# Kernel optimization log

Measured on AMD Instinct MI355X. Metric: run time of the kernel, lower is better.

Reference implementation:

```python
import jax, jax.numpy as jnp
import numpy as np

B, N, H, NH = 2, 2048, 1024, 16
HD = H // NH


def setup_inputs() -> dict:
    key = jax.random.key(0)
    ks = jax.random.split(key, 12)
    s = 0.02
    inp = {
        "q": jax.random.normal(ks[0], (B, N, H), jnp.float32),
        "k": jax.random.normal(ks[1], (B, N, H), jnp.float32),
        "v": jax.random.normal(ks[2], (B, N, H), jnp.float32),
        # causal mask, broadcast over batch and heads
        "mask": jnp.tril(jnp.ones((N, N), jnp.float32))[None, None, :, :],
        "Wq": jax.random.normal(ks[3], (H, H), jnp.float32) * s,
        "bq": jnp.zeros((H,), jnp.float32),
        "Wk": jax.random.normal(ks[4], (H, H), jnp.float32) * s,
        "bk": jnp.zeros((H,), jnp.float32),
        "Wv": jax.random.normal(ks[5], (H, H), jnp.float32) * s,
        "bv": jnp.zeros((H,), jnp.float32),
        "Wp": jax.random.normal(ks[6], (H, H), jnp.float32) * s,
        "bp": jnp.zeros((H,), jnp.float32),
    }
    return inp


def _split_heads(x):
    # [b, n, (h d)] -> [b, h, n, d]
    b, n, _ = x.shape
    return x.reshape(b, n, NH, HD).transpose(0, 2, 1, 3)


def reference(q, k, v, mask, Wq, bq, Wk, bk, Wv, bv, Wp, bp):
    Q = _split_heads(q @ Wq.T + bq)                      # [b,h,n,d]
    K = _split_heads(k @ Wk.T + bk)
    V = _split_heads(v @ Wv.T + bv)
    scores = jnp.einsum("bhnd,bhmd->bhnm", Q, K) / jnp.sqrt(jnp.float32(HD))
    scores = jnp.where(mask == 0, -jnp.inf, scores)
    attn = jax.nn.softmax(scores, axis=-1)
    out = jnp.einsum("bhnm,bhmd->bhnd", attn, V)         # [b,h,n,d]
    out = out.transpose(0, 2, 1, 3).reshape(q.shape[0], q.shape[1], H)
    # dropout is identity in eval mode
    return out @ Wp.T + bp
```

## Files before the change

### kernel.cpp

```cpp
#include <hip/hip_runtime.h>


typedef unsigned short ushortT;
typedef unsigned int uintT;
typedef __attribute__((ext_vector_type(8))) short short8;
typedef __attribute__((ext_vector_type(4))) float f32x4;

#define M_ROWS 4096
#define KDIM   1024
#define NDIM   1024
#define SEQ    2048
#define HDHEAD 64

__device__ __forceinline__ float bf2f(ushortT s) {
    union { unsigned u; float f; } v; v.u = ((unsigned)s) << 16; return v.f;
}
__device__ __forceinline__ ushortT f2bf(float x) {
    union { float f; unsigned u; } v; v.f = x;
    return (ushortT)((v.u + 0x7fffu + ((v.u >> 16) & 1u)) >> 16);
}

__device__ __forceinline__ bool detect_f32(const uintT* w) {
    int hits = 0;
#pragma unroll
    for (int i = 0; i < 16; ++i) {
        const unsigned e = (w[i] >> 7) & 0xffu;
        hits += (e >= 118u && e <= 131u) ? 1 : 0;
    }
    return hits < 8;
}

__device__ __forceinline__ short8 cvt8(const float* p) {
    f32x4 a = *(const f32x4*)p;
    f32x4 b = *(const f32x4*)(p + 4);
    short8 r;
    r[0] = (short)f2bf(a[0]); r[1] = (short)f2bf(a[1]);
    r[2] = (short)f2bf(a[2]); r[3] = (short)f2bf(a[3]);
    r[4] = (short)f2bf(b[0]); r[5] = (short)f2bf(b[1]);
    r[6] = (short)f2bf(b[2]); r[7] = (short)f2bf(b[3]);
    return r;
}

__device__ __forceinline__ void gl2lds16(const ushortT* g, ushortT* l) {
    __builtin_amdgcn_global_load_lds(
        (const __attribute__((address_space(1))) void*)g,
        (__attribute__((address_space(3))) void*)l,
        16, 0, 0);
}

__global__ __launch_bounds__(256) void convert_kernel(
    const void* __restrict__ q, const void* __restrict__ k, const void* __restrict__ v,
    const void* __restrict__ Wq, const void* __restrict__ Wk,
    const void* __restrict__ Wv, const void* __restrict__ Wp,
    const void* __restrict__ bq, const void* __restrict__ bk,
    const void* __restrict__ bv, const void* __restrict__ bp,
    ushortT* __restrict__ dst) {
    const bool f32m = detect_f32((const uintT*)q);
    const size_t u = (size_t)blockIdx.x * 256 + threadIdx.x;

    const void* src; size_t soff, doff;
    if (u < 1572864u) {
        const int seg = (int)(u >> 19);
        const size_t o = u & 524287u;
        src  = seg == 0 ? q : (seg == 1 ? k : v);
        soff = o * 8;
        doff = (size_t)seg * 4194304u + o * 8;
    } else if (u < 2097152u) {
        const size_t u2 = u - 1572864u;
        const int seg = (int)(u2 >> 17);
        const size_t o = u2 & 131071u;
        src  = seg == 0 ? Wq : (seg == 1 ? Wk : (seg == 2 ? Wv : Wp));
        soff = o * 8;
        doff = 12582912u + (size_t)seg * 1048576u + o * 8;
    } else {
        const size_t u3 = u - 2097152u;
        const int seg = (int)(u3 >> 7);
        const size_t o = u3 & 127u;
        src  = seg == 0 ? bq : (seg == 1 ? bk : (seg == 2 ? bv : bp));
        soff = o * 8;
        doff = 16777216u + (size_t)seg * 1024u + o * 8;
    }

    if (f32m)
        *(short8*)(dst + doff) = cvt8((const float*)src + soff);
    else
        *(short8*)(dst + doff) = *(const short8*)((const ushortT*)src + soff);
}

__device__ __forceinline__ void gemm_body(const void* __restrict__ Av,
                                          const void* __restrict__ Wv_,
                                          const void* __restrict__ biasv,
                                          void* __restrict__ Cv,
                                          bool a_f32, bool w_f32, bool c_f32,
                                          float cscale, bool vt_store) {
    __shared__ ushortT ldsA[128 * 64];
    __shared__ ushortT ldsB[128 * 64];

    const int tid  = threadIdx.x;
    const int lane = tid & 63;
    const int wid  = tid >> 6;
    const int bm   = blockIdx.x;
    const int bn   = blockIdx.y;
    const int wm   = wid >> 1;
    const int wn   = wid & 1;

    const int srow = lane >> 2;
    const int scol = (lane & 3) * 8;

    f32x4 acc[4][4];
#pragma unroll
    for (int i = 0; i < 4; ++i)
#pragma unroll
        for (int j = 0; j < 4; ++j) acc[i][j] = (f32x4){0.f, 0.f, 0.f, 0.f};

    const int fr   = lane & 15;
    const int quad = lane >> 4;

    for (int kt = 0; kt < KDIM / 64; ++kt) {
        const int k0 = kt * 64;
        if (!a_f32 && !w_f32) {
#pragma unroll
            for (int t = 0; t < 4; ++t) {
                const int chunk = wid * 4 + t;
                const int kh  = chunk >> 3;
                const int r16 = (chunk & 7) * 16;
                const size_t ra = (size_t)(bm * 128 + r16 + srow) * KDIM + k0 + kh * 32 + scol;
                const size_t rw = (size_t)(bn * 128 + r16 + srow) * KDIM + k0 + kh * 32 + scol;
                gl2lds16((const ushortT*)Av + ra, ldsA + chunk * 512);
                gl2lds16((const ushortT*)Wv_ + rw, ldsB + chunk * 512);
            }
        } else {
            short8 ta[4], tb[4];
#pragma unroll
            for (int t = 0; t < 4; ++t) {
                const int chunk = wid * 4 + t;
                const int kh  = chunk >> 3;
                const int r16 = (chunk & 7) * 16;
                const size_t ra = (size_t)(bm * 128 + r16 + srow) * KDIM + k0 + kh * 32 + scol;
                const size_t rw = (size_t)(bn * 128 + r16 + srow) * KDIM + k0 + kh * 32 + scol;
                ta[t] = a_f32 ? cvt8((const float*)Av + ra)
                              : *(const short8*)((const ushortT*)Av + ra);
                tb[t] = w_f32 ? cvt8((const float*)Wv_ + rw)
                              : *(const short8*)((const ushortT*)Wv_ + rw);
            }
#pragma unroll
            for (int t = 0; t < 4; ++t) {
                const int chunk = wid * 4 + t;
                *(short8*)(ldsA + chunk * 512 + lane * 8) = ta[t];
                *(short8*)(ldsB + chunk * 512 + lane * 8) = tb[t];
            }
        }
        __syncthreads();

#pragma unroll
        for (int s = 0; s < 2; ++s) {
            short8 aF[4], bF[4];
#pragma unroll
            for (int i = 0; i < 4; ++i)
                aF[i] = *(const short8*)(ldsA + s * 4096 + (wm * 64 + i * 16 + fr) * 32 + quad * 8);
#pragma unroll
            for (int j = 0; j < 4; ++j)
                bF[j] = *(const short8*)(ldsB + s * 4096 + (wn * 64 + j * 16 + fr) * 32 + quad * 8);
#pragma unroll
            for (int i = 0; i < 4; ++i)
#pragma unroll
                for (int j = 0; j < 4; ++j)
                    acc[i][j] = __builtin_amdgcn_mfma_f32_16x16x32_bf16(aF[i], bF[j], acc[i][j], 0, 0, 0);
        }
        __syncthreads();
    }

#pragma unroll
    for (int j = 0; j < 4; ++j) {
        const int col = bn * 128 + wn * 64 + j * 16 + fr;
        const float bv = w_f32 ? ((const float*)biasv)[col]
                               : bf2f(((const ushortT*)biasv)[col]);
#pragma unroll
        for (int i = 0; i < 4; ++i) {
            const int row0 = bm * 128 + wm * 64 + i * 16 + quad * 4;
#pragma unroll
            for (int r = 0; r < 4; ++r) {
                const float val = (acc[i][j][r] + bv) * cscale;
                const int row = row0 + r;
                if (vt_store) {
                    const int bb = row >> 11, n = row & 2047;
                    const int hh = col >> 6,  d = col & 63;
                    ((ushortT*)Cv)[(size_t)((bb * 16 + hh) * 64 + d) * SEQ + n] = f2bf(val);
                } else if (c_f32) {
                    ((float*)Cv)[(size_t)row * NDIM + col] = val;
                } else {
                    ((ushortT*)Cv)[(size_t)row * NDIM + col] = f2bf(val);
                }
            }
        }
    }
}

__global__ __launch_bounds__(256, 2) void qkv_proj_kernel(
    const void* __restrict__ q, const void* __restrict__ k, const void* __restrict__ v,
    const void* __restrict__ Wq, const void* __restrict__ Wk, const void* __restrict__ Wv,
    const void* __restrict__ bq, const void* __restrict__ bk, const void* __restrict__ bv,
    ushortT* __restrict__ Qp, ushortT* __restrict__ Kp, ushortT* __restrict__ Vt) {
    const bool f32m = detect_f32((const uintT*)q);
    const void* A; const void* W; const void* bias; ushortT* C;
    float cscale = 1.f; bool vt = false;
    if (blockIdx.z == 0)      { A = q; W = Wq; bias = bq; C = Qp; cscale = 0.125f; }
    else if (blockIdx.z == 1) { A = k; W = Wk; bias = bk; C = Kp; }
    else                      { A = v; W = Wv; bias = bv; C = Vt; vt = true; }
    gemm_body(A, W, bias, (void*)C, f32m, f32m, false, cscale, vt);
}

__global__ __launch_bounds__(256, 2) void out_proj_kernel(
    const ushortT* __restrict__ A, const void* __restrict__ W,
    const void* __restrict__ bias, void* __restrict__ C,
    const void* __restrict__ qdet) {
    const bool wf = detect_f32((const uintT*)W);
    const bool cf = detect_f32((const uintT*)qdet);
    gemm_body((const void*)A, W, bias, C, false, wf, cf, 1.f, false);
}

template <int SPLIT>
__global__ __launch_bounds__(256, SPLIT ? 4 : 2) void flash_attn_kernel(
    const ushortT* __restrict__ Qp, const ushortT* __restrict__ Kp,
    const ushortT* __restrict__ Vt, ushortT* __restrict__ Ob) {
    __shared__ ushortT ldsK[2 * 64 * 40];
    __shared__ ushortT ldsV[64 * 72];
    __shared__ ushortT ldsP[4][16 * 72];

    const int tid  = threadIdx.x;
    const int lane = tid & 63;
    const int wid  = tid >> 6;
    const int fr   = lane & 15;
    const int quad = lane >> 4;

    int pid, sp;
    if constexpr (SPLIT) { pid = blockIdx.x & 15; sp = blockIdx.x >> 4; }
    else                 { pid = blockIdx.x;      sp = 0; }
    const int kstep = SPLIT ? 2 : 1;
    const int h = blockIdx.y;
    const int b = blockIdx.z;

    const size_t base  = (size_t)b * SEQ * NDIM + (size_t)h * HDHEAD;
    const size_t vtb   = (size_t)(b * 16 + h) * HDHEAD * SEQ;

    int ksst[2], keyloc[2];
#pragma unroll
    for (int t = 0; t < 2; ++t) {
        const int chunk = wid * 2 + t;
        ksst[t]   = chunk >> 2;
        keyloc[t] = (chunk & 3) * 16 + (lane >> 2);
    }
    const int c8 = (lane & 3) * 8;
    const int vd  = lane >> 3;
    const int vk8 = (lane & 7) * 8;

    for (int half = 0; half < 2; ++half) {
        const int qb = (half == 0) ? pid : (31 - pid);
        const int q0 = qb * 64;
        const int nkv = qb + 1;

        short8 qf[2];
#pragma unroll
        for (int ks = 0; ks < 2; ++ks)
            qf[ks] = *(const short8*)(Qp + base + (size_t)(q0 + wid * 16 + fr) * NDIM + ks * 32 + quad * 8);

        f32x4 accO[4];
#pragma unroll
        for (int dt = 0; dt < 4; ++dt) accO[dt] = (f32x4){0.f, 0.f, 0.f, 0.f};
        float lsum[4];
#pragma unroll
        for (int r = 0; r < 4; ++r) lsum[r] = 0.f;

        short8 kreg[2], vreg[2];
        const int kvp = sp * 64;
#pragma unroll
        for (int t = 0; t < 2; ++t) {
            kreg[t] = *(const short8*)(Kp + base + (size_t)(kvp + keyloc[t]) * NDIM + ksst[t] * 32 + c8);
            const int d = (wid * 2 + t) * 8 + vd;
            vreg[t] = *(const short8*)(Vt + vtb + (size_t)d * SEQ + kvp + vk8);
        }

        for (int kt = sp; kt < nkv; kt += kstep) {
            __syncthreads();

#pragma unroll
            for (int t = 0; t < 2; ++t) {
                *(short8*)(ldsK + ksst[t] * 2560 + keyloc[t] * 40 + c8) = kreg[t];
                const int d = (wid * 2 + t) * 8 + vd;
                *(short8*)(ldsV + d * 72 + vk8) = vreg[t];
            }

            if (kt + kstep < nkv) {
                const int kv1 = (kt + kstep) * 64;
#pragma unroll
                for (int t = 0; t < 2; ++t) {
                    kreg[t] = *(const short8*)(Kp + base + (size_t)(kv1 + keyloc[t]) * NDIM + ksst[t] * 32 + c8);
                    const int d = (wid * 2 + t) * 8 + vd;
                    vreg[t] = *(const short8*)(Vt + vtb + (size_t)d * SEQ + kv1 + vk8);
                }
            }
            __syncthreads();

            f32x4 s[4];
#pragma unroll
            for (int nt = 0; nt < 4; ++nt) {
                f32x4 a = (f32x4){0.f, 0.f, 0.f, 0.f};
#pragma unroll
                for (int ks = 0; ks < 2; ++ks) {
                    short8 kf = *(const short8*)(ldsK + ks * 2560 + (nt * 16 + fr) * 40 + quad * 8);
                    a = __builtin_amdgcn_mfma_f32_16x16x32_bf16(qf[ks], kf, a, 0, 0, 0);
                }
                s[nt] = a;
            }

            const int kv0 = kt * 64;
            const int qi = q0 + wid * 16 + quad * 4;
            if (kt == nkv - 1) {
#pragma unroll
                for (int nt = 0; nt < 4; ++nt) {
                    const int kj = kv0 + nt * 16 + fr;
#pragma unroll
                    for (int r = 0; r < 4; ++r)
                        s[nt][r] = (kj > qi + r) ? -1e30f : s[nt][r];
                }
            }

            ushortT* pbuf = ldsP[wid];
#pragma unroll
            for (int nt = 0; nt < 4; ++nt) {
#pragma unroll
                for (int r = 0; r < 4; ++r) {
                    const float p = __expf(fminf(s[nt][r], 30.f));
                    lsum[r] += p;
                    pbuf[(quad * 4 + r) * 72 + nt * 16 + fr] = f2bf(p);
                }
            }

            asm volatile("" ::: "memory");

#pragma unroll
            for (int ks = 0; ks < 2; ++ks) {
                short8 pf = *(const short8*)(pbuf + fr * 72 + ks * 32 + quad * 8);
#pragma unroll
                for (int dt = 0; dt < 4; ++dt) {
                    short8 vf = *(const short8*)(ldsV + (dt * 16 + fr) * 72 + ks * 32 + quad * 8);
                    accO[dt] = __builtin_amdgcn_mfma_f32_16x16x32_bf16(pf, vf, accO[dt], 0, 0, 0);
                }
            }
        }

#pragma unroll
        for (int r = 0; r < 4; ++r) {
#pragma unroll
            for (int off = 8; off >= 1; off >>= 1)
                lsum[r] += __shfl_xor(lsum[r], off, 64);
        }

        if constexpr (SPLIT) {
            const size_t pofs = ((size_t)((sp * 2 + b) * 16 + h)) * SEQ * 72;
#pragma unroll
            for (int dt = 0; dt < 4; ++dt) {
#pragma unroll
                for (int r = 0; r < 4; ++r) {
                    const size_t row = (size_t)(q0 + wid * 16 + quad * 4 + r);
                    Ob[pofs + row * 72 + dt * 16 + fr] = f2bf(accO[dt][r]);
                }
            }
            if (fr == 0) {
#pragma unroll
                for (int r = 0; r < 4; ++r) {
                    const size_t row = (size_t)(q0 + wid * 16 + quad * 4 + r);
                    *(float*)(Ob + pofs + row * 72 + 64) = lsum[r];
                }
            }
        } else {
#pragma unroll
            for (int dt = 0; dt < 4; ++dt) {
#pragma unroll
                for (int r = 0; r < 4; ++r) {
                    const size_t row = (size_t)(q0 + wid * 16 + quad * 4 + r);
                    Ob[(size_t)b * SEQ * NDIM + row * NDIM + h * HDHEAD + dt * 16 + fr] =
                        f2bf(accO[dt][r] / lsum[r]);
                }
            }
        }
    }
}

__global__ __launch_bounds__(256) void combine_kernel(
    const ushortT* __restrict__ Part, ushortT* __restrict__ Op) {
    const uintT u = blockIdx.x * 256 + threadIdx.x;
    const int d8  = u & 7;
    const int h   = (u >> 3) & 15;
    const int row = (u >> 7) & 2047;
    const int b   = (int)(u >> 18);

    const size_t r0 = (((size_t)((0 + b) * 16 + h)) * SEQ + row) * 72;
    const size_t r1 = (((size_t)((2 + b) * 16 + h)) * SEQ + row) * 72;
    const short8 p0 = *(const short8*)(Part + r0 + d8 * 8);
    const short8 p1 = *(const short8*)(Part + r1 + d8 * 8);
    const float l = *(const float*)(Part + r0 + 64) + *(const float*)(Part + r1 + 64);
    const float inv = 1.f / l;

    short8 o;
#pragma unroll
    for (int i = 0; i < 8; ++i)
        o[i] = (short)f2bf((bf2f((ushortT)p0[i]) + bf2f((ushortT)p1[i])) * inv);

    Op[((size_t)b * SEQ + row) * NDIM + h * HDHEAD + d8 * 8 + 0] = 0;
    *(short8*)(Op + ((size_t)b * SEQ + row) * NDIM + h * HDHEAD + d8 * 8) = o;
}

extern "C" void kernel_launch(void* const* d_in, const int* in_sizes, int n_in,
                              void* d_out, int out_size, void* d_ws, size_t ws_size,
                              hipStream_t stream) {
    const void* q  = d_in[0];
    const void* k  = d_in[1];
    const void* v  = d_in[2];
    const void* Wq = d_in[4];
    const void* bq = d_in[5];
    const void* Wk = d_in[6];
    const void* bk = d_in[7];
    const void* Wv = d_in[8];
    const void* bv = d_in[9];
    const void* Wp = d_in[10];
    const void* bp = d_in[11];

    dim3 blk(256);
    const size_t FAST_WS = 58728448;

    if (ws_size >= FAST_WS) {
        ushortT* cb   = (ushortT*)d_ws;
        ushortT* qb16 = cb;
        ushortT* kb16 = cb + 4194304u;
        ushortT* vb16 = cb + 8388608u;
        ushortT* Wqb  = cb + 12582912u;
        ushortT* Wkb  = cb + 13631488u;
        ushortT* Wvb  = cb + 14680064u;
        ushortT* Wpb  = cb + 15728640u;
        ushortT* bqb  = cb + 16777216u;
        ushortT* bkb  = cb + 16778240u;
        ushortT* bvb  = cb + 16779264u;
        ushortT* bpb  = cb + 16780288u;
        ushortT* Qp   = cb + 16781312u;
        ushortT* Kp   = Qp + 4194304u;
        ushortT* Vt   = Kp + 4194304u;
        ushortT* Part = cb;
        ushortT* Op   = Vt;

        convert_kernel<<<dim3(8194), blk, 0, stream>>>(
            q, k, v, Wq, Wk, Wv, Wp, bq, bk, bv, bp, cb);
        qkv_proj_kernel<<<dim3(32, 8, 3), blk, 0, stream>>>(
            qb16, kb16, vb16, Wqb, Wkb, Wvb, bqb, bkb, bvb, Qp, Kp, Vt);
        flash_attn_kernel<1><<<dim3(32, 16, 2), blk, 0, stream>>>(Qp, Kp, Vt, Part);
        combine_kernel<<<dim3(2048), blk, 0, stream>>>(Part, Op);
        out_proj_kernel<<<dim3(32, 8), blk, 0, stream>>>(Op, Wpb, bpb, d_out, q);
    } else {
        ushortT* ws = (ushortT*)d_ws;
        ushortT* Qp = ws;
        ushortT* Kp = ws + (size_t)M_ROWS * NDIM;
        ushortT* Vt = ws + (size_t)2 * M_ROWS * NDIM;
        ushortT* Op = ws + (size_t)3 * M_ROWS * NDIM;

        qkv_proj_kernel<<<dim3(32, 8, 3), blk, 0, stream>>>(
            q, k, v, Wq, Wk, Wv, bq, bk, bv, Qp, Kp, Vt);
        flash_attn_kernel<0><<<dim3(16, 16, 2), blk, 0, stream>>>(Qp, Kp, Vt, Op);
        out_proj_kernel<<<dim3(32, 8), blk, 0, stream>>>(Op, Wp, bp, d_out, q);
    }
}
```

Baseline: 247.5 us.

## Compute transposed S tiles per key slice so P stores are vectorized

Each warp now holds one 16-key slice of K and computes S^T against all 64 query rows, so the exponentiated P values pack into 4-wide vector stores into a block-shared P buffer. This replaces the scattered scalar per-warp P writes. It adds a block-wide barrier before the PV product and a cross-warp row-sum reduction through LDS, and each thread now keeps all Q fragments in registers. A redundant scalar store in the combine kernel is also removed.

```diff
diff --git a/kernel.cpp b/kernel.cpp
--- a/kernel.cpp
+++ b/kernel.cpp
@@ -4,6 +4,7 @@
 typedef unsigned short ushortT;
 typedef unsigned int uintT;
 typedef __attribute__((ext_vector_type(8))) short short8;
+typedef __attribute__((ext_vector_type(4))) short short4v;
 typedef __attribute__((ext_vector_type(4))) float f32x4;
 
 #define M_ROWS 4096
@@ -225,7 +226,8 @@
     const ushortT* __restrict__ Vt, ushortT* __restrict__ Ob) {
     __shared__ ushortT ldsK[2 * 64 * 40];
     __shared__ ushortT ldsV[64 * 72];
-    __shared__ ushortT ldsP[4][16 * 72];
+    __shared__ ushortT ldsP[64 * 72];
+    __shared__ float   ldsL[4][64];
 
     const int tid  = threadIdx.x;
     const int lane = tid & 63;
@@ -259,17 +261,19 @@
         const int q0 = qb * 64;
         const int nkv = qb + 1;
 
-        short8 qf[2];
-#pragma unroll
-        for (int ks = 0; ks < 2; ++ks)
-            qf[ks] = *(const short8*)(Qp + base + (size_t)(q0 + wid * 16 + fr) * NDIM + ks * 32 + quad * 8);
+        short8 qf[4][2];
+#pragma unroll
+        for (int i = 0; i < 4; ++i)
+#pragma unroll
+            for (int ks = 0; ks < 2; ++ks)
+                qf[i][ks] = *(const short8*)(Qp + base + (size_t)(q0 + i * 16 + fr) * NDIM + ks * 32 + quad * 8);
 
         f32x4 accO[4];
 #pragma unroll
         for (int dt = 0; dt < 4; ++dt) accO[dt] = (f32x4){0.f, 0.f, 0.f, 0.f};
-        float lsum[4];
-#pragma unroll
-        for (int r = 0; r < 4; ++r) lsum[r] = 0.f;
+        float ls[4];
+#pragma unroll
+        for (int i = 0; i < 4; ++i) ls[i] = 0.f;
 
         short8 kreg[2], vreg[2];
         const int kvp = sp * 64;
@@ -301,46 +305,50 @@
             }
             __syncthreads();
 
-            f32x4 s[4];
-#pragma unroll
-            for (int nt = 0; nt < 4; ++nt) {
+            short8 kf[2];
+#pragma unroll
+            for (int ks = 0; ks < 2; ++ks)
+                kf[ks] = *(const short8*)(ldsK + ks * 2560 + (wid * 16 + fr) * 40 + quad * 8);
+
+            f32x4 st[4];
+#pragma unroll
+            for (int i = 0; i < 4; ++i) {
                 f32x4 a = (f32x4){0.f, 0.f, 0.f, 0.f};
 #pragma unroll
-                for (int ks = 0; ks < 2; ++ks) {
-                    short8 kf = *(const short8*)(ldsK + ks * 2560 + (nt * 16 + fr) * 40 + quad * 8);
-                    a = __builtin_amdgcn_mfma_f32_16x16x32_bf16(qf[ks], kf, a, 0, 0, 0);
-                }
-                s[nt] = a;
+                for (int ks = 0; ks < 2; ++ks)
+                    a = __builtin_amdgcn_mfma_f32_16x16x32_bf16(kf[ks], qf[i][ks], a, 0, 0, 0);
+                st[i] = a;
             }
 
             const int kv0 = kt * 64;
-            const int qi = q0 + wid * 16 + quad * 4;
             if (kt == nkv - 1) {
-#pragma unroll
-                for (int nt = 0; nt < 4; ++nt) {
-                    const int kj = kv0 + nt * 16 + fr;
+                const int kjb = kv0 + wid * 16 + quad * 4;
+#pragma unroll
+                for (int i = 0; i < 4; ++i) {
+                    const int qi = q0 + i * 16 + fr;
 #pragma unroll
                     for (int r = 0; r < 4; ++r)
-                        s[nt][r] = (kj > qi + r) ? -1e30f : s[nt][r];
-                }
-            }
-
-            ushortT* pbuf = ldsP[wid];
-#pragma unroll
-            for (int nt = 0; nt < 4; ++nt) {
+                        st[i][r] = (kjb + r > qi) ? -1e30f : st[i][r];
+                }
+            }
+
+#pragma unroll
+            for (int i = 0; i < 4; ++i) {
+                short4v pk;
 #pragma unroll
                 for (int r = 0; r < 4; ++r) {
-                    const float p = __expf(fminf(s[nt][r], 30.f));
-                    lsum[r] += p;
-                    pbuf[(quad * 4 + r) * 72 + nt * 16 + fr] = f2bf(p);
-                }
-            }
-
-            asm volatile("" ::: "memory");
+                    const float p = __expf(fminf(st[i][r], 30.f));
+                    ls[i] += p;
+                    pk[r] = (short)f2bf(p);
+                }
+                *(short4v*)(ldsP + (i * 16 + fr) * 72 + wid * 16 + quad * 4) = pk;
+            }
+
+            __syncthreads();
 
 #pragma unroll
             for (int ks = 0; ks < 2; ++ks) {
-                short8 pf = *(const short8*)(pbuf + fr * 72 + ks * 32 + quad * 8);
+                short8 pf = *(const short8*)(ldsP + (wid * 16 + fr) * 72 + ks * 32 + quad * 8);
 #pragma unroll
                 for (int dt = 0; dt < 4; ++dt) {
                     short8 vf = *(const short8*)(ldsV + (dt * 16 + fr) * 72 + ks * 32 + quad * 8);
@@ -350,10 +358,23 @@
         }
 
 #pragma unroll
+        for (int i = 0; i < 4; ++i) {
+            ls[i] += __shfl_xor(ls[i], 16, 64);
+            ls[i] += __shfl_xor(ls[i], 32, 64);
+        }
+        __syncthreads();
+        if (lane < 16) {
+#pragma unroll
+            for (int i = 0; i < 4; ++i)
+                ldsL[wid][i * 16 + lane] = ls[i];
+        }
+        __syncthreads();
+
+        float ltot[4];
+#pragma unroll
         for (int r = 0; r < 4; ++r) {
-#pragma unroll
-            for (int off = 8; off >= 1; off >>= 1)
-                lsum[r] += __shfl_xor(lsum[r], off, 64);
+            const int qrow = wid * 16 + quad * 4 + r;
+            ltot[r] = ldsL[0][qrow] + ldsL[1][qrow] + ldsL[2][qrow] + ldsL[3][qrow];
         }
 
         if constexpr (SPLIT) {
@@ -370,7 +391,7 @@
 #pragma unroll
                 for (int r = 0; r < 4; ++r) {
                     const size_t row = (size_t)(q0 + wid * 16 + quad * 4 + r);
-                    *(float*)(Ob + pofs + row * 72 + 64) = lsum[r];
+                    *(float*)(Ob + pofs + row * 72 + 64) = ltot[r];
                 }
             }
         } else {
@@ -380,10 +401,11 @@
                 for (int r = 0; r < 4; ++r) {
                     const size_t row = (size_t)(q0 + wid * 16 + quad * 4 + r);
                     Ob[(size_t)b * SEQ * NDIM + row * NDIM + h * HDHEAD + dt * 16 + fr] =
-                        f2bf(accO[dt][r] / lsum[r]);
-                }
-            }
-        }
+                        f2bf(accO[dt][r] / ltot[r]);
+                }
+            }
+        }
+        __syncthreads();
     }
 }
 
@@ -407,7 +429,6 @@
     for (int i = 0; i < 8; ++i)
         o[i] = (short)f2bf((bf2f((ushortT)p0[i]) + bf2f((ushortT)p1[i])) * inv);
 
-    Op[((size_t)b * SEQ + row) * NDIM + h * HDHEAD + d8 * 8 + 0] = 0;
     *(short8*)(Op + ((size_t)b * SEQ + row) * NDIM + h * HDHEAD + d8 * 8) = o;
 }
 
```

New measurement: 250.5 us. About the same (+1.2%).

## Fuse split-KV combine into output projection GEMM A-tile load

Applied to the files above, without the earlier changes.

Removes the separate combine kernel and instead merges the two split-attention partial outputs, normalising by the summed row sums, while loading A tiles inside a new output projection GEMM kernel. This saves one launch and the write and re-read of the combined attention output. The trade-off is that each of the 8 N-blocks recomputes the combine for its rows, so partial buffers are read 8 times. The A operand is also now staged through registers rather than via direct global-to-LDS loads, and the loop has no double buffering.

```diff
diff --git a/kernel.cpp b/kernel.cpp
--- a/kernel.cpp
+++ b/kernel.cpp
@@ -219,6 +219,105 @@
     gemm_body((const void*)A, W, bias, C, false, wf, cf, 1.f, false);
 }
 
+__global__ __launch_bounds__(256, 2) void out_proj_combined(
+    const ushortT* __restrict__ Part, const ushortT* __restrict__ W,
+    const ushortT* __restrict__ bias, void* __restrict__ C,
+    const void* __restrict__ qdet) {
+    __shared__ ushortT ldsA[128 * 64];
+    __shared__ ushortT ldsB[128 * 64];
+
+    const bool cf = detect_f32((const uintT*)qdet);
+
+    const int tid  = threadIdx.x;
+    const int lane = tid & 63;
+    const int wid  = tid >> 6;
+    const int bm   = blockIdx.x;
+    const int bn   = blockIdx.y;
+    const int wm   = wid >> 1;
+    const int wn   = wid & 1;
+
+    const int srow = lane >> 2;
+    const int scol = (lane & 3) * 8;
+
+    f32x4 acc[4][4];
+#pragma unroll
+    for (int i = 0; i < 4; ++i)
+#pragma unroll
+        for (int j = 0; j < 4; ++j) acc[i][j] = (f32x4){0.f, 0.f, 0.f, 0.f};
+
+    const int fr   = lane & 15;
+    const int quad = lane >> 4;
+
+    for (int kt = 0; kt < KDIM / 64; ++kt) {
+        const int k0 = kt * 64;
+        short8 ta[4];
+#pragma unroll
+        for (int t = 0; t < 4; ++t) {
+            const int chunk = wid * 4 + t;
+            const int kh   = chunk >> 3;
+            const int r16  = (chunk & 7) * 16;
+            const int row  = bm * 128 + r16 + srow;
+            const int bb   = row >> 11;
+            const int row2 = row & 2047;
+            const int c    = k0 + kh * 32 + scol;
+            const int hh   = c >> 6, d = c & 63;
+            const size_t rb0 = (((size_t)(bb * 16 + hh)) * SEQ + row2) * 72;
+            const size_t rb1 = (((size_t)((2 + bb) * 16 + hh)) * SEQ + row2) * 72;
+            const short8 p0 = *(const short8*)(Part + rb0 + d);
+            const short8 p1 = *(const short8*)(Part + rb1 + d);
+            const float l = *(const float*)(Part + rb0 + 64)
+                          + *(const float*)(Part + rb1 + 64);
+            const float inv = 1.f / l;
+            short8 o;
+#pragma unroll
+            for (int i = 0; i < 8; ++i)
+                o[i] = (short)f2bf((bf2f((ushortT)p0[i]) + bf2f((ushortT)p1[i])) * inv);
+            ta[t] = o;
+
+            const size_t rw = (size_t)(bn * 128 + r16 + srow) * KDIM + k0 + kh * 32 + scol;
+            gl2lds16(W + rw, ldsB + chunk * 512);
+        }
+#pragma unroll
+        for (int t = 0; t < 4; ++t)
+            *(short8*)(ldsA + (wid * 4 + t) * 512 + lane * 8) = ta[t];
+        __syncthreads();
+
+#pragma unroll
+        for (int s = 0; s < 2; ++s) {
+            short8 aF[4], bF[4];
+#pragma unroll
+            for (int i = 0; i < 4; ++i)
+                aF[i] = *(const short8*)(ldsA + s * 4096 + (wm * 64 + i * 16 + fr) * 32 + quad * 8);
+#pragma unroll
+            for (int j = 0; j < 4; ++j)
+                bF[j] = *(const short8*)(ldsB + s * 4096 + (wn * 64 + j * 16 + fr) * 32 + quad * 8);
+#pragma unroll
+            for (int i = 0; i < 4; ++i)
+#pragma unroll
+                for (int j = 0; j < 4; ++j)
+                    acc[i][j] = __builtin_amdgcn_mfma_f32_16x16x32_bf16(aF[i], bF[j], acc[i][j], 0, 0, 0);
+        }
+        __syncthreads();
+    }
+
+#pragma unroll
+    for (int j = 0; j < 4; ++j) {
+        const int col = bn * 128 + wn * 64 + j * 16 + fr;
+        const float bv = bf2f(bias[col]);
+#pragma unroll
+        for (int i = 0; i < 4; ++i) {
+            const int row0 = bm * 128 + wm * 64 + i * 16 + quad * 4;
+#pragma unroll
+            for (int r = 0; r < 4; ++r) {
+                const float val = acc[i][j][r] + bv;
+                const int row = row0 + r;
+                if (cf) ((float*)C)[(size_t)row * NDIM + col] = val;
+                else    ((ushortT*)C)[(size_t)row * NDIM + col] = f2bf(val);
+            }
+        }
+    }
+}
+
 template <int SPLIT>
 __global__ __launch_bounds__(256, SPLIT ? 4 : 2) void flash_attn_kernel(
     const ushortT* __restrict__ Qp, const ushortT* __restrict__ Kp,
@@ -385,30 +484,6 @@
             }
         }
     }
-}
-
-__global__ __launch_bounds__(256) void combine_kernel(
-    const ushortT* __restrict__ Part, ushortT* __restrict__ Op) {
-    const uintT u = blockIdx.x * 256 + threadIdx.x;
-    const int d8  = u & 7;
-    const int h   = (u >> 3) & 15;
-    const int row = (u >> 7) & 2047;
-    const int b   = (int)(u >> 18);
-
-    const size_t r0 = (((size_t)((0 + b) * 16 + h)) * SEQ + row) * 72;
-    const size_t r1 = (((size_t)((2 + b) * 16 + h)) * SEQ + row) * 72;
-    const short8 p0 = *(const short8*)(Part + r0 + d8 * 8);
-    const short8 p1 = *(const short8*)(Part + r1 + d8 * 8);
-    const float l = *(const float*)(Part + r0 + 64) + *(const float*)(Part + r1 + 64);
-    const float inv = 1.f / l;
-
-    short8 o;
-#pragma unroll
-    for (int i = 0; i < 8; ++i)
-        o[i] = (short)f2bf((bf2f((ushortT)p0[i]) + bf2f((ushortT)p1[i])) * inv);
-
-    Op[((size_t)b * SEQ + row) * NDIM + h * HDHEAD + d8 * 8 + 0] = 0;
-    *(short8*)(Op + ((size_t)b * SEQ + row) * NDIM + h * HDHEAD + d8 * 8) = o;
 }
 
 extern "C" void kernel_launch(void* const* d_in, const int* in_sizes, int n_in,
@@ -446,15 +521,13 @@
         ushortT* Kp   = Qp + 4194304u;
         ushortT* Vt   = Kp + 4194304u;
         ushortT* Part = cb;
-        ushortT* Op   = Vt;
 
         convert_kernel<<<dim3(8194), blk, 0, stream>>>(
             q, k, v, Wq, Wk, Wv, Wp, bq, bk, bv, bp, cb);
         qkv_proj_kernel<<<dim3(32, 8, 3), blk, 0, stream>>>(
             qb16, kb16, vb16, Wqb, Wkb, Wvb, bqb, bkb, bvb, Qp, Kp, Vt);
         flash_attn_kernel<1><<<dim3(32, 16, 2), blk, 0, stream>>>(Qp, Kp, Vt, Part);
-        combine_kernel<<<dim3(2048), blk, 0, stream>>>(Part, Op);
-        out_proj_kernel<<<dim3(32, 8), blk, 0, stream>>>(Op, Wpb, bpb, d_out, q);
+        out_proj_combined<<<dim3(32, 8), blk, 0, stream>>>(Part, Wpb, bpb, d_out, q);
     } else {
         ushortT* ws = (ushortT*)d_ws;
         ushortT* Qp = ws;
```

Measured after the change: 261.7 us. +5.7%, slower.
